# Kernel tuning notes

Hardware: AMD Instinct MI355X
Metric: run time of the kernel (lower is better)

The kernel has to match this reference:

```python
import jax, jax.numpy as jnp
import numpy as np

# dims: batch, seq_len, d_model, heads, head_dim, n_buckets
B, L, DM, H, DH, K = 4, 4096, 1024, 16, 64, 8
C = L // K            # chunk length after bucket sort (512); extra_len==0 for these dims
CS = 0.1              # cluster_score mixing weight


def setup_inputs() -> dict:
    key = jax.random.key(0)
    ks = jax.random.split(key, 12)
    s = 0.02
    def p(k, shape):
        return jax.random.normal(k, shape, jnp.float32) * s
    return {
        "inputs_q": jax.random.normal(ks[0], (B, L, DM), jnp.float32),
        "wq": p(ks[1], (DM, H, DH)), "bq": jnp.zeros((H, DH), jnp.float32),
        "wk": p(ks[2], (DM, H, DH)), "bk": jnp.zeros((H, DH), jnp.float32),
        "wv": p(ks[3], (DM, H, DH)), "bv": jnp.zeros((H, DH), jnp.float32),
        "w_shared": p(ks[4], (H, DH, K)),
        "w_qscore": p(ks[5], (H, DH, K)),
        "w_kscore": p(ks[6], (H, DH, K)),
        "wo": p(ks[7], (H, DH, DM)), "bo": jnp.zeros((DM,), jnp.float32),
    }


def reference(inputs_q, wq, bq, wk, bk, wv, bv, w_shared, w_qscore, w_kscore, wo, bo):
    scale = 1.0 / np.sqrt(DH)
    # QKV projections (DenseGeneral to (H, DH))
    q = jnp.einsum('bld,dhk->blhk', inputs_q, wq) + bq  # [B,L,H,DH]
    k = jnp.einsum('bld,dhk->blhk', inputs_q, wk) + bk
    v = jnp.einsum('bld,dhk->blhk', inputs_q, wv) + bv

    # learned linear cluster scores on stop-gradient q/k
    mix_q = (1.0 - CS) * w_shared + CS * w_qscore  # [H,DH,K]
    mix_k = (1.0 - CS) * w_shared + CS * w_kscore
    qs = jnp.einsum('blhd,hdk->blhk', jax.lax.stop_gradient(q), mix_q)  # [B,L,H,K]
    ksc = jnp.einsum('blhd,hdk->blhk', jax.lax.stop_gradient(k), mix_k)

    # bucket assignment = argmax learned score; per-(batch,head) stable sort by bucket id
    bq_id = jnp.argmax(qs, -1).transpose(0, 2, 1)   # [B,H,L]
    bk_id = jnp.argmax(ksc, -1).transpose(0, 2, 1)
    sort_q = jnp.argsort(bq_id, axis=-1)            # stable in jax
    sort_k = jnp.argsort(bk_id, axis=-1)

    qh = q.transpose(0, 2, 1, 3)  # [B,H,L,DH]
    kh = k.transpose(0, 2, 1, 3)
    vh = v.transpose(0, 2, 1, 3)
    sq = jnp.take_along_axis(qh, sort_q[..., None], axis=2).reshape(B, H, K, C, DH)
    sk = jnp.take_along_axis(kh, sort_k[..., None], axis=2).reshape(B, H, K, C, DH)
    sv = jnp.take_along_axis(vh, sort_k[..., None], axis=2).reshape(B, H, K, C, DH)

    # block attention within each bucket chunk
    logits = jnp.einsum('bhncd,bhned->bhnce', sq, sk) * scale  # [B,H,K,C,C]
    attn = jax.nn.softmax(logits, axis=-1)
    o = jnp.einsum('bhnce,bhned->bhncd', attn, sv).reshape(B, H, L, DH)

    # unsort back to original token order
    inv_q = jnp.argsort(sort_q, axis=-1)
    o = jnp.take_along_axis(o, inv_q[..., None], axis=2)  # [B,H,L,DH]
    o = o.transpose(0, 2, 1, 3)                            # [B,L,H,DH]

    out = jnp.einsum('blhd,hdo->blo', o, wo) + bo          # output projection

    # auxiliary load-balancing routing loss over buckets (extra_loss)
    p_q = jax.nn.softmax(qs, -1)
    p_k = jax.nn.softmax(ksc, -1)
    f_q = jax.nn.one_hot(jnp.argmax(qs, -1), K, dtype=qs.dtype)
    f_k = jax.nn.one_hot(jnp.argmax(ksc, -1), K, dtype=qs.dtype)
    lq = K * jnp.mean(jnp.sum(jnp.mean(f_q, 1) * jnp.mean(p_q, 1), -1))
    lk = K * jnp.mean(jnp.sum(jnp.mean(f_k, 1) * jnp.mean(p_k, 1), -1))
    extra_loss = 0.5 * (lq + lk)
    return out, extra_loss
```

## Files before the change

### kernel.cpp

```cpp
#include <hip/hip_runtime.h>
#include <hip/hip_bf16.h>

#define BB 4
#define LL 4096
#define DM 1024
#define HH 16
#define DHD 64
#define KB 8
#define BL 16384
#define FLAGCAP 131072

typedef __attribute__((ext_vector_type(8))) short short8;
typedef __attribute__((ext_vector_type(4))) short short4v;
typedef __attribute__((ext_vector_type(4))) float float4v;

#define MFMA16(A, Bx, C) __builtin_amdgcn_mfma_f32_16x16x32_bf16(A, Bx, C, 0, 0, 0)

static __device__ __forceinline__ short bf16s(float f) {
  __hip_bfloat16 h = __float2bfloat16(f);
  return *reinterpret_cast<short*>(&h);
}
static __device__ __forceinline__ float b2f(short s) {
  __hip_bfloat16 h = *reinterpret_cast<__hip_bfloat16*>(&s);
  return __bfloat162float(h);
}
static __device__ __forceinline__ void gl16(const void* g, void* l) {
  __builtin_amdgcn_global_load_lds(
      (const __attribute__((address_space(1))) void*)g,
      (__attribute__((address_space(3))) void*)l, 16, 0, 0);
}

__global__ __launch_bounds__(256) void prep_wt(const float* __restrict__ wq,
                                               const float* __restrict__ wk,
                                               const float* __restrict__ wv,
                                               const float* __restrict__ wo,
                                               __hip_bfloat16* __restrict__ wt_qkv,
                                               __hip_bfloat16* __restrict__ wt_o) {
  int blk = blockIdx.x;
  int s = blk >> 8;
  int rem = blk & 255;
  int k0 = (rem >> 4) * 64;
  int n0 = (rem & 15) * 64;
  const float* src = (s == 0) ? wq : (s == 1) ? wk : (s == 2) ? wv : wo;
  __hip_bfloat16* dst = (s < 3) ? (wt_qkv + (size_t)s * 1024 * 1024) : wt_o;
  __shared__ float ls[64][65];
  int t = threadIdx.x;
#pragma unroll
  for (int p = 0; p < 4; ++p) {
    int sid = p * 256 + t;
    int r = sid >> 4, c4 = sid & 15;
    float4 v = *reinterpret_cast<const float4*>(src + (size_t)(k0 + r) * 1024 + n0 + c4 * 4);
    ls[r][c4 * 4 + 0] = v.x; ls[r][c4 * 4 + 1] = v.y;
    ls[r][c4 * 4 + 2] = v.z; ls[r][c4 * 4 + 3] = v.w;
  }
  __syncthreads();
#pragma unroll
  for (int p = 0; p < 4; ++p) {
    int sid = p * 256 + t;
    int n = sid >> 4, kq = sid & 15;
    short4v pk;
#pragma unroll
    for (int j = 0; j < 4; ++j) pk[j] = bf16s(ls[kq * 4 + j][n]);
    *reinterpret_cast<short4v*>(dst + (size_t)(n0 + n) * 1024 + k0 + kq * 4) = pk;
  }
}

__global__ __launch_bounds__(256) void prep_wsc(const float* __restrict__ wq,
                                                const float* __restrict__ wk,
                                                const float* __restrict__ wsh,
                                                const float* __restrict__ wqs,
                                                const float* __restrict__ wks,
                                                const float* __restrict__ bq,
                                                const float* __restrict__ bk,
                                                double* __restrict__ wscg,
                                                double* __restrict__ bsc,
                                                __hip_bfloat16* __restrict__ whb,
                                                __hip_bfloat16* __restrict__ wmb) {
  int col = blockIdx.x;
  int side = col >> 7, h = (col >> 3) & 15, kk = col & 7;
  int g = side * 16 + h;
  const float* w = side ? wk : wq;
  const float* wscore = side ? wks : wqs;
  __shared__ double mix[64];
  int t = threadIdx.x;
  if (t < 64)
    mix[t] = 0.9 * (double)wsh[(h * 64 + t) * 8 + kk] +
             0.1 * (double)wscore[(h * 64 + t) * 8 + kk];
  __syncthreads();
#pragma unroll
  for (int p = 0; p < 4; ++p) {
    int d = p * 256 + t;
    double acc = 0.0;
    const float* wr = w + (size_t)d * 1024 + h * 64;
#pragma unroll
    for (int j = 0; j < 64; ++j) acc += (double)wr[j] * mix[j];
    wscg[((size_t)g * 1024 + d) * 8 + kk] = acc;
    short hi = bf16s((float)acc);
    short mid = bf16s((float)(acc - (double)b2f(hi)));
    *reinterpret_cast<short*>(whb + (size_t)col * 1024 + d) = hi;
    *reinterpret_cast<short*>(wmb + (size_t)col * 1024 + d) = mid;
  }
  if (t == 0) {
    const float* br = (side ? bk : bq) + h * 64;
    double acc = 0.0;
    for (int j = 0; j < 64; ++j) acc += (double)br[j] * mix[j];
    bsc[col] = acc;
  }
}

__global__ __launch_bounds__(256) void score_gemm(const float* __restrict__ x,
                                                  const __hip_bfloat16* __restrict__ whb,
                                                  const __hip_bfloat16* __restrict__ wmb,
                                                  const double* __restrict__ bsc,
                                                  __hip_bfloat16* __restrict__ xb,
                                                  int* __restrict__ bid,
                                                  float* __restrict__ psumg,
                                                  int* __restrict__ flagcnt,
                                                  int* __restrict__ list) {
  __shared__ char sm[49152];
  int t = threadIdx.x;
  int m0 = blockIdx.x * 64;
  int n0 = blockIdx.y * 128;
  int lane = t & 63;
  int wu = __builtin_amdgcn_readfirstlane(t >> 6);
  int lm = lane & 15, quad = lane >> 4;
  int wmr = (wu & 1) * 32, wn = (wu >> 1) * 64;
  int rb = wu * 32, rr = lane >> 3, phys = lane & 7;
  float4v zero = {0.f, 0.f, 0.f, 0.f};
  float4v acc[2][4];
#pragma unroll
  for (int i = 0; i < 2; ++i)
#pragma unroll
    for (int j = 0; j < 4; ++j) acc[i][j] = zero;

  for (int k0 = 0; k0 < 1024; k0 += 64) {
    __syncthreads();
#pragma unroll
    for (int p = 0; p < 2; ++p) {
      int sid = p * 256 + t;
      int m = sid >> 3, kc = sid & 7;
      const float* ap = x + (size_t)(m0 + m) * 1024 + k0 + kc * 8;
      float4 f0 = *reinterpret_cast<const float4*>(ap);
      float4 f1 = *reinterpret_cast<const float4*>(ap + 4);
      float vv[8] = {f0.x, f0.y, f0.z, f0.w, f1.x, f1.y, f1.z, f1.w};
      short8 hi, lo;
#pragma unroll
      for (int e = 0; e < 8; ++e) {
        short h = bf16s(vv[e]);
        hi[e] = h;
        lo[e] = bf16s(vv[e] - b2f(h));
      }
      *reinterpret_cast<short8*>(sm + m * 128 + ((kc + m) & 7) * 16) = hi;
      *reinterpret_cast<short8*>(sm + 8192 + m * 128 + ((kc + m) & 7) * 16) = lo;
      if (blockIdx.y == 0)
        *reinterpret_cast<short8*>(xb + (size_t)(m0 + m) * 1024 + k0 + kc * 8) = hi;
    }
#pragma unroll
    for (int p = 0; p < 4; ++p) {
      int row = rb + p * 8 + rr;
      int kc = (phys - row) & 7;
      gl16(whb + (size_t)(n0 + row) * 1024 + k0 + kc * 8, sm + 16384 + (rb + p * 8) * 128);
      gl16(wmb + (size_t)(n0 + row) * 1024 + k0 + kc * 8, sm + 32768 + (rb + p * 8) * 128);
    }
    __syncthreads();
#pragma unroll
    for (int kh = 0; kh < 2; ++kh) {
      short8 ah[2], al[2], bh[4], bm[4];
#pragma unroll
      for (int i = 0; i < 2; ++i) {
        int row = wmr + i * 16 + lm;
        int ph = ((kh * 4 + quad) + row) & 7;
        ah[i] = *reinterpret_cast<const short8*>(sm + row * 128 + ph * 16);
        al[i] = *reinterpret_cast<const short8*>(sm + 8192 + row * 128 + ph * 16);
      }
#pragma unroll
      for (int j = 0; j < 4; ++j) {
        int rn = wn + j * 16 + lm;
        int ph = ((kh * 4 + quad) + rn) & 7;
        bh[j] = *reinterpret_cast<const short8*>(sm + 16384 + rn * 128 + ph * 16);
        bm[j] = *reinterpret_cast<const short8*>(sm + 32768 + rn * 128 + ph * 16);
      }
#pragma unroll
      for (int i = 0; i < 2; ++i)
#pragma unroll
        for (int j = 0; j < 4; ++j) {
          acc[i][j] = MFMA16(ah[i], bh[j], acc[i][j]);
          acc[i][j] = MFMA16(ah[i], bm[j], acc[i][j]);
          acc[i][j] = MFMA16(al[i], bh[j], acc[i][j]);
        }
    }
  }

  int b = m0 >> 12;
  int l0 = m0 & 4095;
  int kk = lm & 7;
#pragma unroll
  for (int j = 0; j < 4; ++j) {
    int n = n0 + wn + j * 16 + lm;
    int g = n >> 3;
    int side = g >> 4, h = g & 15;
    int slab = (side * 4 + b) * 16 + h;
    float bias = (float)bsc[n];
    float pp = 0.f;
#pragma unroll
    for (int i = 0; i < 2; ++i)
#pragma unroll
      for (int r = 0; r < 4; ++r) {
        float v = acc[i][j][r] + bias;
        float bmx = v; int bi = kk;
#pragma unroll
        for (int o = 1; o < 8; o <<= 1) {
          float vo = __shfl_xor(bmx, o);
          int io = __shfl_xor(bi, o);
          if (vo > bmx || (vo == bmx && io < bi)) { bmx = vo; bi = io; }
        }
        float vm = (kk == bi) ? -3.0e38f : v;
#pragma unroll
        for (int o = 1; o < 8; o <<= 1) vm = fmaxf(vm, __shfl_xor(vm, o));
        float e = __expf(v - bmx);
        float es = e;
#pragma unroll
        for (int o = 1; o < 8; o <<= 1) es += __shfl_xor(es, o);
        pp += e * (1.f / es);
        int l = l0 + wmr + i * 16 + quad * 4 + r;
        if (kk == 0) {
          bid[(slab << 12) | l] = bi;
          if (bmx - vm < 5e-4f) {
            int pos = atomicAdd(flagcnt, 1);
            if (pos < FLAGCAP) list[pos] = (slab << 12) | l;
          }
        }
      }
    pp += __shfl_xor(pp, 16);
    pp += __shfl_xor(pp, 32);
    if (quad == 0) atomicAdd(&psumg[slab * 8 + kk], pp);
  }
}

__global__ __launch_bounds__(256) void refine_kernel(const float* __restrict__ x,
                                                     const double* __restrict__ wscg,
                                                     const double* __restrict__ bsc,
                                                     const int* __restrict__ flagcnt,
                                                     const int* __restrict__ list,
                                                     int* __restrict__ bid) {
  int lane = threadIdx.x & 63;
  int w = threadIdx.x >> 6;
  int cnt = flagcnt[0];
  if (cnt > FLAGCAP) cnt = FLAGCAP;
  for (int i = blockIdx.x * 4 + w; i < cnt; i += 1024) {
    int e = list[i];
    int slab = e >> 12, l = e & 4095;
    int side = slab >> 6, b = (slab >> 4) & 3, h = slab & 15;
    int g = side * 16 + h;
    int row = b * 4096 + l;
    double acc[8] = {0, 0, 0, 0, 0, 0, 0, 0};
    const float* xr = x + (size_t)row * 1024 + lane * 16;
    const double* wr = wscg + ((size_t)g * 1024 + lane * 16) * 8;
#pragma unroll
    for (int dd = 0; dd < 16; ++dd) {
      double xv = (double)xr[dd];
#pragma unroll
      for (int j = 0; j < 8; ++j) acc[j] += xv * wr[dd * 8 + j];
    }
#pragma unroll
    for (int j = 0; j < 8; ++j) {
      double v = acc[j];
      v += __shfl_xor(v, 32); v += __shfl_xor(v, 16); v += __shfl_xor(v, 8);
      v += __shfl_xor(v, 4);  v += __shfl_xor(v, 2);  v += __shfl_xor(v, 1);
      acc[j] = v + bsc[g * 8 + j];
    }
    if (lane == 0) {
      double mx = acc[0]; int am = 0;
#pragma unroll
      for (int j = 1; j < 8; ++j) { if (acc[j] > mx) { mx = acc[j]; am = j; } }
      bid[(slab << 12) | l] = am;
    }
  }
}

__global__ __launch_bounds__(256) void sort_kernel(const int* __restrict__ bid,
                                                   int* __restrict__ sortq,
                                                   int* __restrict__ sortk,
                                                   int* __restrict__ cntg) {
  int blk = blockIdx.x;
  int side = blk >> 6, b = (blk >> 4) & 3, h = blk & 15;
  const int* ids = bid + (((side * 4 + b) * 16 + h) << 12);
  int* outp = (side ? sortk : sortq) + ((b * 16 + h) << 12);
  __shared__ int cnt[8][257];
  __shared__ int base[8];
  int t = threadIdx.x;
  int loc[16];
  int hist[8] = {0, 0, 0, 0, 0, 0, 0, 0};
#pragma unroll
  for (int j = 0; j < 16; ++j) { loc[j] = ids[t * 16 + j] & 7; hist[loc[j]]++; }
#pragma unroll
  for (int k = 0; k < 8; ++k) cnt[k][t + 1] = hist[k];
  if (t < 8) cnt[t][0] = 0;
  __syncthreads();
  if (t < 8) {
    for (int i = 1; i <= 256; ++i) cnt[t][i] += cnt[t][i - 1];
  }
  __syncthreads();
  if (t == 0) {
    int run = 0;
    for (int k = 0; k < 8; ++k) { base[k] = run; run += cnt[k][256]; }
  }
  if (t < 8) cntg[((side * 4 + b) * 16 + h) * 8 + t] = cnt[t][256];
  __syncthreads();
#pragma unroll
  for (int j = 0; j < 16; ++j) {
    int k = loc[j];
    int before = 0;
#pragma unroll
    for (int i = 0; i < 16; ++i) before += (i < j && loc[i] == k) ? 1 : 0;
    int pos = base[k] + cnt[k][t] + before;
    outp[pos] = t * 16 + j;
  }
}

template <bool CBF16>
__global__ __launch_bounds__(512, 2) void gemm256(const __hip_bfloat16* __restrict__ A,
                                                  const __hip_bfloat16* __restrict__ Bt,
                                                  void* __restrict__ Cv,
                                                  const float* __restrict__ b0,
                                                  const float* __restrict__ b1,
                                                  const float* __restrict__ b2,
                                                  int nblk, int cpx) {
  __shared__ char sm[131072];
  int t = threadIdx.x;
  int blk = (blockIdx.x & 7) * cpx + (blockIdx.x >> 3);
  int m0 = (blk / nblk) * 256;
  int n0 = (blk % nblk) * 256;
  int lane = t & 63;
  int wu = __builtin_amdgcn_readfirstlane(t >> 6);
  int lm = lane & 15, quad = lane >> 4;
  int rr = lane >> 3, phys = lane & 7;
  int wrow = (wu & 1) * 64;
  int wcol = (wu >> 1) * 32;

  constexpr int QM[4] = {0, 0, 1, 1};
  constexpr int QN[4] = {0, 1, 1, 0};

  auto STAGE = [&](char* bufn, int j, int kS) {
    const int mat = (j == 1 || j == 2) ? 1 : 0;
    const int hm = (j >= 2) ? 1 : 0;
    const __hip_bfloat16* src = mat ? Bt : A;
    int gb = mat ? n0 : m0;
    char* lb = bufn + mat * 32768 + hm * 16384;
#pragma unroll
    for (int i = 0; i < 2; ++i) {
      int r = hm * 128 + (wu * 2 + i) * 8 + rr;
      int kc = (phys - r) & 7;
      gl16(src + (size_t)(gb + r) * 1024 + kS + kc * 8, lb + (wu * 2 + i) * 1024);
    }
  };

#pragma unroll
  for (int j = 0; j < 4; ++j) STAGE(sm, j, 0);

  float4v zero = {0.f, 0.f, 0.f, 0.f};
  float4v acc[4][4][2];
#pragma unroll
  for (int q = 0; q < 4; ++q)
#pragma unroll
    for (int mi = 0; mi < 4; ++mi)
#pragma unroll
      for (int ni = 0; ni < 2; ++ni) acc[q][mi][ni] = zero;

  short8 a[4][2], b[2][2];
  auto READA = [&](const char* bc, int qm) {
#pragma unroll
    for (int mi = 0; mi < 4; ++mi) {
      int row = qm * 128 + wrow + mi * 16 + lm;
#pragma unroll
      for (int ks = 0; ks < 2; ++ks) {
        int ph = ((ks * 4 + quad) + row) & 7;
        a[mi][ks] = *reinterpret_cast<const short8*>(bc + row * 128 + ph * 16);
      }
    }
  };
  auto READB = [&](const char* bc, int qn) {
#pragma unroll
    for (int ni = 0; ni < 2; ++ni) {
      int rn = qn * 128 + wcol + ni * 16 + lm;
#pragma unroll
      for (int ks = 0; ks < 2; ++ks) {
        int ph = ((ks * 4 + quad) + rn) & 7;
        b[ni][ks] = *reinterpret_cast<const short8*>(bc + 32768 + rn * 128 + ph * 16);
      }
    }
  };

#pragma unroll 1
  for (int kt = 0; kt < 16; ++kt) {
    char* bc = sm + ((kt & 1) << 16);
    char* bn = sm + (((kt & 1) ^ 1) << 16);
    int kS = (kt < 15) ? (kt + 1) * 64 : 960;
#pragma unroll
    for (int j = 0; j < 4; ++j) {
      if (j < 3) {
        asm volatile("s_waitcnt vmcnt(4)" ::: "memory");
        __builtin_amdgcn_s_barrier();
      }
      if (j == 0) { READA(bc, 0); READB(bc, 0); }
      else if (j == 1) { READB(bc, 1); }
      else if (j == 2) { READA(bc, 1); }
      else { READB(bc, 0); }
      STAGE(bn, j, kS);
      __builtin_amdgcn_s_setprio(1);
#pragma unroll
      for (int mi = 0; mi < 4; ++mi)
#pragma unroll
        for (int ni = 0; ni < 2; ++ni)
#pragma unroll
          for (int ks = 0; ks < 2; ++ks)
            acc[j][mi][ni] = MFMA16(a[mi][ks], b[ni][ks], acc[j][mi][ni]);
      __builtin_amdgcn_s_setprio(0);
    }
  }
  asm volatile("s_waitcnt vmcnt(0)" ::: "memory");

  if constexpr (CBF16) {
#pragma unroll
    for (int j = 0; j < 4; ++j)
#pragma unroll
      for (int mi = 0; mi < 4; ++mi)
#pragma unroll
        for (int ni = 0; ni < 2; ++ni) {
          int nn = n0 + QN[j] * 128 + wcol + ni * 16 + lm;
          int s = nn >> 10, nnb = nn & 1023;
          const float* bias = (s == 0) ? b0 : (s == 1) ? b1 : b2;
          float bvx = bias[nnb];
          __hip_bfloat16* C = (__hip_bfloat16*)Cv + (size_t)s * BL * 1024;
#pragma unroll
          for (int r = 0; r < 4; ++r) {
            int row = m0 + QM[j] * 128 + wrow + mi * 16 + quad * 4 + r;
            C[(size_t)row * 1024 + nnb] = __float2bfloat16(acc[j][mi][ni][r] + bvx);
          }
        }
  } else {
    float* C = (float*)Cv;
#pragma unroll
    for (int j = 0; j < 4; ++j)
#pragma unroll
      for (int mi = 0; mi < 4; ++mi)
#pragma unroll
        for (int ni = 0; ni < 2; ++ni) {
          int nn = n0 + QN[j] * 128 + wcol + ni * 16 + lm;
          float bvx = b0[nn];
#pragma unroll
          for (int r = 0; r < 4; ++r) {
            int row = m0 + QM[j] * 128 + wrow + mi * 16 + quad * 4 + r;
            C[(size_t)row * 1024 + nn] = acc[j][mi][ni][r] + bvx;
          }
        }
  }
}

__global__ __launch_bounds__(256) void vt_kernel(const __hip_bfloat16* __restrict__ vb,
                                                 const int* __restrict__ sortk,
                                                 __hip_bfloat16* __restrict__ vT) {
  int cid = blockIdx.x;
  int b = cid >> 7, h = (cid >> 3) & 15, n = cid & 7;
  int sbase = ((b * 16 + h) << 12) + n * 512;
  __shared__ __hip_bfloat16 ls[64][72];
  int t = threadIdx.x;
  for (int kt = 0; kt < 8; ++kt) {
    __syncthreads();
#pragma unroll
    for (int p = 0; p < 2; ++p) {
      int sid = p * 256 + t;
      int key = sid >> 3, kc = sid & 7;
      int tok = sortk[sbase + kt * 64 + key];
      short8 v = *reinterpret_cast<const short8*>(vb + ((size_t)(b * 4096 + tok) * 16 + h) * 64 + kc * 8);
      *reinterpret_cast<short8*>(&ls[key][kc * 8]) = v;
    }
    __syncthreads();
#pragma unroll
    for (int p = 0; p < 2; ++p) {
      int sid = p * 256 + t;
      int dim = sid >> 3, kc = sid & 7;
      short8 o;
#pragma unroll
      for (int j = 0; j < 8; ++j) o[j] = *reinterpret_cast<short*>(&ls[kc * 8 + j][dim]);
      *reinterpret_cast<short8*>(vT + ((size_t)cid * 64 + dim) * 512 + kt * 64 + kc * 8) = o;
    }
  }
}

__global__ __launch_bounds__(256) void attn_kernel(const __hip_bfloat16* __restrict__ qb,
                                                   const __hip_bfloat16* __restrict__ kb,
                                                   const __hip_bfloat16* __restrict__ vT,
                                                   const int* __restrict__ sortq,
                                                   const int* __restrict__ sortk,
                                                   __hip_bfloat16* __restrict__ ao) {
  __shared__ char sm[25600];
  int t = threadIdx.x;
  int lane = t & 63, w = t >> 6;
  int lm = lane & 15, quad = lane >> 4;
  int cid = blockIdx.x >> 3, qt = blockIdx.x & 7;
  int b = cid >> 7, h = (cid >> 3) & 15, n = cid & 7;
  int sbase = (b * 16 + h) << 12;
  int psOff = 16384 + w * 2304;

  int qtok = sortq[sbase + n * 512 + qt * 64 + w * 16 + lm];
  const __hip_bfloat16* qp = qb + ((size_t)(b * 4096 + qtok) * 16 + h) * 64 + quad * 8;
  short8 aq0 = *reinterpret_cast<const short8*>(qp);
  short8 aq1 = *reinterpret_cast<const short8*>(qp + 32);

  float4v zero = {0.f, 0.f, 0.f, 0.f};
  float4v accO[4];
#pragma unroll
  for (int i = 0; i < 4; ++i) accO[i] = zero;
  float lsum[4] = {0.f, 0.f, 0.f, 0.f};

  for (int kt = 0; kt < 8; ++kt) {
    __syncthreads();
#pragma unroll
    for (int p = 0; p < 2; ++p) {
      int sid = p * 256 + t;
      int row = sid >> 3, kc = sid & 7;
      int tok = sortk[sbase + n * 512 + kt * 64 + row];
      short8 kv = *reinterpret_cast<const short8*>(kb + ((size_t)(b * 4096 + tok) * 16 + h) * 64 + kc * 8);
      *reinterpret_cast<short8*>(sm + row * 128 + ((kc + row) & 7) * 16) = kv;
      short8 vv = *reinterpret_cast<const short8*>(vT + ((size_t)cid * 64 + row) * 512 + kt * 64 + kc * 8);
      *reinterpret_cast<short8*>(sm + 8192 + row * 128 + ((kc + row) & 7) * 16) = vv;
    }
    __syncthreads();
#pragma unroll
    for (int nt = 0; nt < 4; ++nt) {
      int key = nt * 16 + lm;
      int ph0 = (quad + key) & 7;
      int ph1 = (4 + quad + key) & 7;
      short8 bk0 = *reinterpret_cast<const short8*>(sm + key * 128 + ph0 * 16);
      short8 bk1 = *reinterpret_cast<const short8*>(sm + key * 128 + ph1 * 16);
      float4v S = zero;
      S = MFMA16(aq0, bk0, S);
      S = MFMA16(aq1, bk1, S);
#pragma unroll
      for (int r = 0; r < 4; ++r) {
        float e = __expf(S[r] * 0.125f);
        lsum[r] += e;
        *reinterpret_cast<short*>(sm + psOff + (quad * 4 + r) * 144 + key * 2) = bf16s(e);
      }
    }
    __builtin_amdgcn_s_waitcnt(0);
#pragma unroll
    for (int ks = 0; ks < 2; ++ks) {
      short8 ap = *reinterpret_cast<const short8*>(sm + psOff + lm * 144 + ks * 64 + quad * 16);
#pragma unroll
      for (int dt = 0; dt < 4; ++dt) {
        int dim = dt * 16 + lm;
        int ph = (ks * 4 + quad + dim) & 7;
        short8 bv = *reinterpret_cast<const short8*>(sm + 8192 + dim * 128 + ph * 16);
        accO[dt] = MFMA16(ap, bv, accO[dt]);
      }
    }
  }
#pragma unroll
  for (int r = 0; r < 4; ++r) {
    float l = lsum[r];
    l += __shfl_xor(l, 1); l += __shfl_xor(l, 2);
    l += __shfl_xor(l, 4); l += __shfl_xor(l, 8);
    lsum[r] = 1.f / l;
  }
#pragma unroll
  for (int dt = 0; dt < 4; ++dt)
#pragma unroll
    for (int r = 0; r < 4; ++r)
      *reinterpret_cast<short*>(sm + psOff + (quad * 4 + r) * 144 + (dt * 16 + lm) * 2) =
          bf16s(accO[dt][r] * lsum[r]);
  __builtin_amdgcn_s_waitcnt(0);
  int q2 = lane >> 2, c = lane & 3;
  int tok2 = sortq[sbase + n * 512 + qt * 64 + w * 16 + q2];
  __hip_bfloat16* op = ao + ((size_t)(b * 4096 + tok2) * 16 + h) * 64;
  short8 o0 = *reinterpret_cast<const short8*>(sm + psOff + q2 * 144 + c * 16);
  short8 o1 = *reinterpret_cast<const short8*>(sm + psOff + q2 * 144 + (c + 4) * 16);
  *reinterpret_cast<short8*>(op + c * 8) = o0;
  *reinterpret_cast<short8*>(op + (c + 4) * 8) = o1;
}

__global__ __launch_bounds__(1024) void loss_kernel(const int* __restrict__ cntg,
                                                    const float* __restrict__ psumg,
                                                    float* __restrict__ out) {
  int t = threadIdx.x;
  float term = ((float)cntg[t] * (1.f / 4096.f)) * (psumg[t] * (1.f / 4096.f));
#pragma unroll
  for (int o = 1; o < 64; o <<= 1) term += __shfl_xor(term, o);
  __shared__ float wsum[16];
  if ((t & 63) == 0) wsum[t >> 6] = term;
  __syncthreads();
  if (t == 0) {
    float s = 0.f;
    for (int i = 0; i < 16; ++i) s += wsum[i];
    out[16777216] = s * (1.f / 16.f);
  }
}

extern "C" void kernel_launch(void* const* d_in, const int* in_sizes, int n_in,
                              void* d_out, int out_size, void* d_ws, size_t ws_size,
                              hipStream_t stream) {
  (void)in_sizes; (void)n_in; (void)out_size; (void)ws_size;
  const float* x   = (const float*)d_in[0];
  const float* wq  = (const float*)d_in[1];
  const float* bq  = (const float*)d_in[2];
  const float* wk  = (const float*)d_in[3];
  const float* bk  = (const float*)d_in[4];
  const float* wv  = (const float*)d_in[5];
  const float* bv  = (const float*)d_in[6];
  const float* wsh = (const float*)d_in[7];
  const float* wqs = (const float*)d_in[8];
  const float* wks = (const float*)d_in[9];
  const float* wo  = (const float*)d_in[10];
  const float* bo  = (const float*)d_in[11];

  char* ws = (char*)d_ws;
  __hip_bfloat16* wt_qkv = (__hip_bfloat16*)(ws + 0);
  __hip_bfloat16* wt_o   = (__hip_bfloat16*)(ws + 6291456);
  double* wscg  = (double*)(ws + 8388608);
  double* bsc   = (double*)(ws + 10485760);
  __hip_bfloat16* qkv  = (__hip_bfloat16*)(ws + 10487808);
  __hip_bfloat16* whb = (__hip_bfloat16*)(ws + 109051904);
  __hip_bfloat16* wmb = (__hip_bfloat16*)(ws + 109576192);
  int* flagcnt = (int*)(ws + 110100480);
  int* list    = (int*)(ws + 110100736);
  __hip_bfloat16* attn = (__hip_bfloat16*)(ws + 111151104);
  int* bid    = (int*)(ws + 144705536);
  int* sortq  = (int*)(ws + 146802688);
  int* sortk  = (int*)(ws + 147851264);
  float* psumg = (float*)(ws + 148899840);
  int* cntg    = (int*)(ws + 148903936);
  __hip_bfloat16* vT = (__hip_bfloat16*)d_out;
  __hip_bfloat16* xb = (__hip_bfloat16*)((char*)d_out + 33554432);
  float* out = (float*)d_out;

  hipMemsetAsync(psumg, 0, 8192, stream);
  hipMemsetAsync(flagcnt, 0, 4, stream);
  prep_wt<<<1024, 256, 0, stream>>>(wq, wk, wv, wo, wt_qkv, wt_o);
  prep_wsc<<<256, 256, 0, stream>>>(wq, wk, wsh, wqs, wks, bq, bk, wscg, bsc, whb, wmb);
  score_gemm<<<dim3(256, 2), 256, 0, stream>>>(x, whb, wmb, bsc, xb, bid, psumg, flagcnt, list);
  refine_kernel<<<256, 256, 0, stream>>>(x, wscg, bsc, flagcnt, list, bid);
  sort_kernel<<<128, 256, 0, stream>>>(bid, sortq, sortk, cntg);
  gemm256<true><<<768, 512, 0, stream>>>(xb, wt_qkv, qkv, bq, bk, bv, 12, 96);
  vt_kernel<<<512, 256, 0, stream>>>(qkv + (size_t)2 * BL * 1024, sortk, vT);
  attn_kernel<<<4096, 256, 0, stream>>>(qkv, qkv + (size_t)BL * 1024, vT, sortq, sortk, attn);
  gemm256<false><<<256, 512, 0, stream>>>(attn, wt_o, (void*)out, bo, bo, bo, 4, 32);
  loss_kernel<<<1, 1024, 0, stream>>>(cntg, psumg, out);
}
```

Measured before the change: 538.3 us.

## Double-buffer weight tiles and prefetch x in score_gemm main loop

Software-pipelines the score_gemm K loop. The next weight tile is staged into an alternate LDS buffer and the next x slice is prefetched into registers while the current tile is being consumed. Explicit waitcnt and barrier instructions replace the two __syncthreads per iteration. This hides global-load latency behind MFMA work, at the cost of more LDS (80KB), which may reduce occupancy, and more registers.

```diff
diff --git a/kernel.cpp b/kernel.cpp
--- a/kernel.cpp
+++ b/kernel.cpp
@@ -117,7 +117,7 @@
                                                   float* __restrict__ psumg,
                                                   int* __restrict__ flagcnt,
                                                   int* __restrict__ list) {
-  __shared__ char sm[49152];
+  __shared__ char sm[81920];
   int t = threadIdx.x;
   int m0 = blockIdx.x * 64;
   int n0 = blockIdx.y * 128;
@@ -126,43 +126,79 @@
   int lm = lane & 15, quad = lane >> 4;
   int wmr = (wu & 1) * 32, wn = (wu >> 1) * 64;
   int rb = wu * 32, rr = lane >> 3, phys = lane & 7;
-  float4v zero = {0.f, 0.f, 0.f, 0.f};
-  float4v acc[2][4];
-#pragma unroll
-  for (int i = 0; i < 2; ++i)
-#pragma unroll
-    for (int j = 0; j < 4; ++j) acc[i][j] = zero;
-
-  for (int k0 = 0; k0 < 1024; k0 += 64) {
-    __syncthreads();
+
+  auto STAGEB = [&](int bufsel, int k0) {
+    char* base = sm + 16384 + bufsel * 32768;
+#pragma unroll
+    for (int p = 0; p < 4; ++p) {
+      int row = rb + p * 8 + rr;
+      int kc = (phys - row) & 7;
+      gl16(whb + (size_t)(n0 + row) * 1024 + k0 + kc * 8, base + (rb + p * 8) * 128);
+      gl16(wmb + (size_t)(n0 + row) * 1024 + k0 + kc * 8, base + 16384 + (rb + p * 8) * 128);
+    }
+  };
+
+  float4 xf[2][2];
+  auto LOADX = [&](int k0) {
 #pragma unroll
     for (int p = 0; p < 2; ++p) {
       int sid = p * 256 + t;
       int m = sid >> 3, kc = sid & 7;
       const float* ap = x + (size_t)(m0 + m) * 1024 + k0 + kc * 8;
-      float4 f0 = *reinterpret_cast<const float4*>(ap);
-      float4 f1 = *reinterpret_cast<const float4*>(ap + 4);
-      float vv[8] = {f0.x, f0.y, f0.z, f0.w, f1.x, f1.y, f1.z, f1.w};
-      short8 hi, lo;
+      xf[p][0] = *reinterpret_cast<const float4*>(ap);
+      xf[p][1] = *reinterpret_cast<const float4*>(ap + 4);
+    }
+  };
+
+  STAGEB(0, 0);
+  LOADX(0);
+
+  float4v zero = {0.f, 0.f, 0.f, 0.f};
+  float4v acc[2][4];
+#pragma unroll
+  for (int i = 0; i < 2; ++i)
+#pragma unroll
+    for (int j = 0; j < 4; ++j) acc[i][j] = zero;
+
+#pragma unroll 1
+  for (int kt = 0; kt < 16; ++kt) {
+    int k0 = kt * 64;
+    short8 hi[2], lo[2];
+#pragma unroll
+    for (int p = 0; p < 2; ++p) {
+      float vv[8] = {xf[p][0].x, xf[p][0].y, xf[p][0].z, xf[p][0].w,
+                     xf[p][1].x, xf[p][1].y, xf[p][1].z, xf[p][1].w};
 #pragma unroll
       for (int e = 0; e < 8; ++e) {
         short h = bf16s(vv[e]);
-        hi[e] = h;
-        lo[e] = bf16s(vv[e] - b2f(h));
-      }
-      *reinterpret_cast<short8*>(sm + m * 128 + ((kc + m) & 7) * 16) = hi;
-      *reinterpret_cast<short8*>(sm + 8192 + m * 128 + ((kc + m) & 7) * 16) = lo;
+        hi[p][e] = h;
+        lo[p][e] = bf16s(vv[e] - b2f(h));
+      }
+    }
+    asm volatile("" ::: "memory");
+    __builtin_amdgcn_s_barrier();
+    asm volatile("" ::: "memory");
+#pragma unroll
+    for (int p = 0; p < 2; ++p) {
+      int sid = p * 256 + t;
+      int m = sid >> 3, kc = sid & 7;
+      *reinterpret_cast<short8*>(sm + m * 128 + ((kc + m) & 7) * 16) = hi[p];
+      *reinterpret_cast<short8*>(sm + 8192 + m * 128 + ((kc + m) & 7) * 16) = lo[p];
       if (blockIdx.y == 0)
-        *reinterpret_cast<short8*>(xb + (size_t)(m0 + m) * 1024 + k0 + kc * 8) = hi;
-    }
-#pragma unroll
-    for (int p = 0; p < 4; ++p) {
-      int row = rb + p * 8 + rr;
-      int kc = (phys - row) & 7;
-      gl16(whb + (size_t)(n0 + row) * 1024 + k0 + kc * 8, sm + 16384 + (rb + p * 8) * 128);
-      gl16(wmb + (size_t)(n0 + row) * 1024 + k0 + kc * 8, sm + 32768 + (rb + p * 8) * 128);
-    }
-    __syncthreads();
+        *reinterpret_cast<short8*>(xb + (size_t)(m0 + m) * 1024 + k0 + kc * 8) = hi[p];
+    }
+    if (kt < 15) {
+      STAGEB((kt + 1) & 1, k0 + 64);
+      LOADX(k0 + 64);
+      asm volatile("s_waitcnt vmcnt(12)" ::: "memory");
+    } else {
+      asm volatile("s_waitcnt vmcnt(0)" ::: "memory");
+    }
+    asm volatile("s_waitcnt lgkmcnt(0)" ::: "memory");
+    __builtin_amdgcn_s_barrier();
+    asm volatile("" ::: "memory");
+
+    const char* bb = sm + 16384 + (kt & 1) * 32768;
 #pragma unroll
     for (int kh = 0; kh < 2; ++kh) {
       short8 ah[2], al[2], bh[4], bm[4];
@@ -177,8 +213,8 @@
       for (int j = 0; j < 4; ++j) {
         int rn = wn + j * 16 + lm;
         int ph = ((kh * 4 + quad) + rn) & 7;
-        bh[j] = *reinterpret_cast<const short8*>(sm + 16384 + rn * 128 + ph * 16);
-        bm[j] = *reinterpret_cast<const short8*>(sm + 32768 + rn * 128 + ph * 16);
+        bh[j] = *reinterpret_cast<const short8*>(bb + rn * 128 + ph * 16);
+        bm[j] = *reinterpret_cast<const short8*>(bb + 16384 + rn * 128 + ph * 16);
       }
 #pragma unroll
       for (int i = 0; i < 2; ++i)
```

Result: faster. 520.2 us (-3.4%).
